# Kernel optimization log

Measured on AMD Instinct MI355X. Metric: run time of the kernel, lower is better.

The kernel has to match this reference:

```python
import jax, jax.numpy as jnp
import numpy as np

K = 1          # self.k: number of hardest positives kept per row
MARGIN = 0.1   # self.margin


def setup_inputs() -> dict:
    key = jax.random.key(0)
    n, d, n_classes = 8192, 512, 1024  # 8 samples per class (balanced, as the torch reshape assumes)
    inputs = jax.random.normal(key, (n, d), dtype=jnp.float32)
    targets = (jnp.arange(n) % n_classes).astype(jnp.int32)
    return {"inputs": inputs, "targets": targets}


def _euclidean_dist(x):
    # ||xi||^2 + ||xj||^2 - 2 xi.xj, clamped then sqrt (matches torch addmm_ version)
    sq = jnp.sum(x * x, axis=1)
    d2 = sq[:, None] + sq[None, :] - 2.0 * (x @ x.T)
    return jnp.sqrt(jnp.clip(d2, 1e-12))


def reference(inputs, targets):
    n = inputs.shape[0]
    dist = _euclidean_dist(inputs)                      # [n, n]

    same = targets[:, None] == targets[None, :]
    eye = jnp.eye(n, dtype=bool)
    pos_mask = same & ~eye                              # same label, excl. diagonal
    neg_mask = ~same                                    # different label

    inf = jnp.asarray(jnp.inf, dist.dtype)
    # per-row sorted positive distances (non-positives pushed to +inf)
    pos_sorted = jnp.sort(jnp.where(pos_mask, dist, inf), axis=1)
    topk_pos = pos_sorted[:, :K]                        # k closest positives per row
    mean_pos = jnp.mean(topk_pos, axis=1)               # mean(pos_pair[:k])
    thresh = pos_sorted[:, K - 1] + MARGIN              # pos_pair[-1] + margin

    # hard negatives: neg distance < threshold
    sel = neg_mask & (dist < thresh[:, None])
    cnt = jnp.sum(sel, axis=1)
    sum_neg = jnp.sum(jnp.where(sel, dist, 0.0), axis=1)
    mean_neg = sum_neg / jnp.maximum(cnt, 1).astype(dist.dtype)

    valid = cnt > 0
    row_loss = jnp.where(valid, mean_pos - mean_neg + MARGIN, 0.0)
    loss = jnp.sum(row_loss) / n

    prec = 1.0 - jnp.sum(valid).astype(dist.dtype) / n
    pos_d = jnp.sum(jnp.where(pos_mask, dist, 0.0)) / jnp.sum(pos_mask).astype(dist.dtype)
    neg_d = jnp.sum(jnp.where(neg_mask, dist, 0.0)) / jnp.sum(neg_mask).astype(dist.dtype)
    return loss, prec, pos_d, neg_d
```

## Files before the change

### kernel.cpp

```cpp
#include <hip/hip_runtime.h>
#include <hip/hip_bf16.h>
#include <math.h>


#define MARGIN_F 0.1f

typedef unsigned short ushort_t;
typedef __attribute__((ext_vector_type(8))) _Float16 f16x8;
typedef __attribute__((ext_vector_type(4))) float f32x4;

__global__ void nl_prep_kernel(const float* __restrict__ x, float* __restrict__ sq,
                               ushort_t* __restrict__ xh,
                               float* __restrict__ neg_total, unsigned int* __restrict__ neg_cnt,
                               int n, int d) {
  int row = blockIdx.x * blockDim.y + threadIdx.y;
  if (row >= n) return;
  const float* xr = x + (size_t)row * d;
  float s = 0.f;
  for (int k = threadIdx.x * 4; k < d; k += 64 * 4) {
    float4 v = *reinterpret_cast<const float4*>(xr + k);
    s = fmaf(v.x, v.x, s); s = fmaf(v.y, v.y, s);
    s = fmaf(v.z, v.z, s); s = fmaf(v.w, v.w, s);
    if (xh != nullptr) {
      float f[4] = {v.x, v.y, v.z, v.w};
      union { ushort_t u[4]; uint2 v2; } H;
#pragma unroll
      for (int t = 0; t < 4; ++t) {
        _Float16 h = (_Float16)f[t];
        H.u[t] = *reinterpret_cast<ushort_t*>(&h);
      }
      *reinterpret_cast<uint2*>(xh + (size_t)row * d + k) = H.v2;
    }
  }
#pragma unroll
  for (int off = 32; off > 0; off >>= 1) s += __shfl_down(s, off, 64);
  if (threadIdx.x == 0) sq[row] = s;
  if (row == 0 && threadIdx.x == 0) { *neg_total = 0.f; *neg_cnt = 0u; }
}

__launch_bounds__(1024)
__global__ void nl_bucket_kernel(const int* __restrict__ targets,
                                 int* __restrict__ cls_start, int* __restrict__ members,
                                 int n) {
  __shared__ int cnt[8192];
  __shared__ int aux[1024];
  const int tid = threadIdx.x;
  for (int k = tid; k < n; k += 1024) cnt[k] = 0;
  __syncthreads();
  for (int k = tid; k < n; k += 1024) atomicAdd(&cnt[targets[k]], 1);
  __syncthreads();
  const int C = (n + 1023) / 1024;
  int v[8]; int s = 0;
  for (int e = 0; e < C; ++e) {
    int idx = tid * C + e;
    int t = (idx < n) ? cnt[idx] : 0;
    v[e] = s; s += t;
  }
  aux[tid] = s;
  __syncthreads();
  for (int off = 1; off < 1024; off <<= 1) {
    int t = (tid >= off) ? aux[tid - off] : 0;
    __syncthreads();
    aux[tid] += t;
    __syncthreads();
  }
  int chunk_excl = aux[tid] - s;
  __syncthreads();
  for (int e = 0; e < C; ++e) {
    int idx = tid * C + e;
    if (idx < n) {
      int st = chunk_excl + v[e];
      cls_start[idx] = st;
      cnt[idx] = st;
    }
  }
  __syncthreads();
  for (int k = tid; k < n; k += 1024) {
    int t = targets[k];
    int p = atomicAdd(&cnt[t], 1);
    members[p] = k;
  }
}

__launch_bounds__(256)
__global__ void nl_pos_bucket(const float* __restrict__ x, const int* __restrict__ targets,
                              const float* __restrict__ sq,
                              const int* __restrict__ cls_start, const int* __restrict__ members,
                              float* __restrict__ min_pos, float* __restrict__ pos_sum,
                              int* __restrict__ pos_cnt,
                              float* __restrict__ sel_sum, int* __restrict__ sel_cnt,
                              int n, int d) {
  const int lane = threadIdx.x & 63;
  const int i = (blockIdx.x * blockDim.x + threadIdx.x) >> 6;
  if (i >= n) return;
  const int tgt = targets[i];
  const float sqi = sq[i];
  const float* xi = x + (size_t)i * d;
  float4 xreg[2];
  const int k0 = lane * 4;
#pragma unroll
  for (int c = 0; c < 2; ++c)
    if (k0 + c * 256 < d) xreg[c] = *reinterpret_cast<const float4*>(xi + k0 + c * 256);
  const int s = cls_start[tgt];
  const int e = (tgt + 1 < n) ? cls_start[tgt + 1] : n;
  float mn = INFINITY, sum = 0.f;
  int cnt = 0;
  for (int mi = s; mi < e; ++mi) {
    int j = members[mi];
    if (j == i) continue;
    const float* xj = x + (size_t)j * d;
    float acc = 0.f;
    if (d == 512) {
      float4 a0 = xreg[0], a1 = xreg[1];
      float4 v0 = *reinterpret_cast<const float4*>(xj + k0);
      float4 v1 = *reinterpret_cast<const float4*>(xj + k0 + 256);
      acc = fmaf(a0.x, v0.x, acc); acc = fmaf(a0.y, v0.y, acc);
      acc = fmaf(a0.z, v0.z, acc); acc = fmaf(a0.w, v0.w, acc);
      acc = fmaf(a1.x, v1.x, acc); acc = fmaf(a1.y, v1.y, acc);
      acc = fmaf(a1.z, v1.z, acc); acc = fmaf(a1.w, v1.w, acc);
    } else {
      for (int k = k0; k < d; k += 256) {
        float4 a = *reinterpret_cast<const float4*>(xi + k);
        float4 v = *reinterpret_cast<const float4*>(xj + k);
        acc = fmaf(a.x, v.x, acc); acc = fmaf(a.y, v.y, acc);
        acc = fmaf(a.z, v.z, acc); acc = fmaf(a.w, v.w, acc);
      }
    }
#pragma unroll
    for (int off = 32; off > 0; off >>= 1) acc += __shfl_down(acc, off, 64);
    if (lane == 0) {
      float d2 = sqi + sq[j] - 2.f * acc;
      float dist = sqrtf(fmaxf(d2, 1e-12f));
      mn = fminf(mn, dist); sum += dist; cnt++;
    }
  }
  if (lane == 0) {
    min_pos[i] = mn; pos_sum[i] = sum; pos_cnt[i] = cnt;
    sel_sum[i] = 0.f; sel_cnt[i] = 0;
  }
}

__launch_bounds__(256)
__global__ void nl_pos_scan(const float* __restrict__ x, const int* __restrict__ targets,
                            const float* __restrict__ sq,
                            float* __restrict__ min_pos, float* __restrict__ pos_sum,
                            int* __restrict__ pos_cnt,
                            float* __restrict__ sel_sum, int* __restrict__ sel_cnt,
                            int n, int d) {
  const int lane = threadIdx.x & 63;
  const int i = (blockIdx.x * blockDim.x + threadIdx.x) >> 6;
  if (i >= n) return;
  const int tgt = targets[i];
  const float sqi = sq[i];
  const float* xi = x + (size_t)i * d;
  float mn = INFINITY, sum = 0.f;
  int cnt = 0;
  for (int j0 = 0; j0 < n; j0 += 64) {
    int j = j0 + lane;
    bool match = (j < n) && (j != i) && (targets[j] == tgt);
    unsigned long long mask = __ballot(match);
    while (mask) {
      int b = __ffsll(mask) - 1;
      mask &= mask - 1;
      int jj = j0 + b;
      const float* xj = x + (size_t)jj * d;
      float acc = 0.f;
      for (int k = lane * 4; k < d; k += 256) {
        float4 a = *reinterpret_cast<const float4*>(xi + k);
        float4 v = *reinterpret_cast<const float4*>(xj + k);
        acc = fmaf(a.x, v.x, acc); acc = fmaf(a.y, v.y, acc);
        acc = fmaf(a.z, v.z, acc); acc = fmaf(a.w, v.w, acc);
      }
#pragma unroll
      for (int off = 32; off > 0; off >>= 1) acc += __shfl_down(acc, off, 64);
      if (lane == 0) {
        float d2 = sqi + sq[jj] - 2.f * acc;
        float dist = sqrtf(fmaxf(d2, 1e-12f));
        mn = fminf(mn, dist); sum += dist; cnt++;
      }
    }
  }
  if (lane == 0) {
    min_pos[i] = mn; pos_sum[i] = sum; pos_cnt[i] = cnt;
    sel_sum[i] = 0.f; sel_cnt[i] = 0;
  }
}

__device__ __forceinline__ void stage_tile(const ushort_t* __restrict__ S, int r0, int k0,
                                           int ld, char* lds) {
  const int tid = threadIdx.x;
#pragma unroll
  for (int i = 0; i < 2; ++i) {
    int c = tid + i * 256;
    int row = c >> 2;
    int kc = (c & 3) ^ ((row >> 1) & 3);
    const ushort_t* g = S + (size_t)(r0 + row) * ld + k0 + kc * 8;
    __builtin_amdgcn_global_load_lds(
        (const __attribute__((address_space(1))) unsigned int*)g,
        (__attribute__((address_space(3))) unsigned int*)(lds + c * 16),
        16, 0, 0);
  }
}

__launch_bounds__(256, 4)
__global__ void nl_main_mfma(const ushort_t* __restrict__ xh,
                             const int* __restrict__ targets, const float* __restrict__ sq,
                             const float* __restrict__ min_pos,
                             float* __restrict__ sel_sum, int* __restrict__ sel_cnt,
                             float* __restrict__ neg_total, unsigned int* __restrict__ neg_cnt,
                             int n, int d) {
  __shared__ char smem[2][2][8192];
  __shared__ float red_sel[128];
  __shared__ int red_cnt[128];
  __shared__ float red_csel[128];
  __shared__ int red_ccnt[128];
  __shared__ float red_neg;
  __shared__ unsigned int red_negc;

  const int tid = threadIdx.x;
  const int lane = tid & 63;
  const int w = tid >> 6;
  const int wr = (w >> 1) & 1, wc = w & 1;

  const int nwg = gridDim.x;
  const int q8 = nwg >> 3, r8 = nwg & 7;
  const int xcd = blockIdx.x & 7, sub = blockIdx.x >> 3;
  const int wg = (xcd < r8 ? xcd * (q8 + 1) : r8 * (q8 + 1) + (xcd - r8) * q8) + sub;

  const int nbx = n >> 7;
  int tt = wg, bi = 0, len = nbx;
  while (tt >= len) { tt -= len; ++bi; --len; }
  const int bj = bi + tt;
  const int row0 = bi * 128, col0 = bj * 128;
  const bool isdiag = (bi == bj);

  if (tid < 128) { red_sel[tid] = 0.f; red_cnt[tid] = 0; red_csel[tid] = 0.f; red_ccnt[tid] = 0; }
  if (tid == 0) { red_neg = 0.f; red_negc = 0u; }

  f32x4 acc[4][4];
#pragma unroll
  for (int m = 0; m < 4; ++m)
#pragma unroll
    for (int nn = 0; nn < 4; ++nn) acc[m][nn] = (f32x4){0.f, 0.f, 0.f, 0.f};

  const int TOT = d >> 5;

  stage_tile(xh, row0, 0, d, smem[0][0]);
  stage_tile(xh, col0, 0, d, smem[0][1]);

  const int r = lane & 15;
  const int g = lane >> 4;
  const int chunk = (g ^ ((r >> 1) & 3)) * 16;

  for (int kt = 0; kt < TOT; ++kt) {
    __builtin_amdgcn_s_barrier();
    __builtin_amdgcn_sched_barrier(0);
    if (kt + 1 < TOT) {
      int k0 = (kt + 1) << 5;
      stage_tile(xh, row0, k0, d, smem[(kt + 1) & 1][0]);
      stage_tile(xh, col0, k0, d, smem[(kt + 1) & 1][1]);
      asm volatile("s_waitcnt vmcnt(4)" ::: "memory");
    } else {
      asm volatile("s_waitcnt vmcnt(0)" ::: "memory");
    }
    __builtin_amdgcn_s_barrier();
    __builtin_amdgcn_sched_barrier(0);

    const char* As = smem[kt & 1][0];
    const char* Bs = smem[kt & 1][1];
    f16x8 a[4], b[4];
#pragma unroll
    for (int m = 0; m < 4; ++m)
      a[m] = *reinterpret_cast<const f16x8*>(As + (wr * 64 + m * 16 + r) * 64 + chunk);
#pragma unroll
    for (int nn = 0; nn < 4; ++nn)
      b[nn] = *reinterpret_cast<const f16x8*>(Bs + (wc * 64 + nn * 16 + r) * 64 + chunk);
#pragma unroll
    for (int m = 0; m < 4; ++m)
#pragma unroll
      for (int nn = 0; nn < 4; ++nn)
        acc[m][nn] = __builtin_amdgcn_mfma_f32_16x16x32_f16(a[m], b[nn], acc[m][nn], 0, 0, 0);
  }

  const int col_base = col0 + wc * 64;
  float sqj[4], thrj[4];
  int tgtj[4];
#pragma unroll
  for (int nn = 0; nn < 4; ++nn) {
    int gc = col_base + nn * 16 + (lane & 15);
    sqj[nn] = sq[gc];
    tgtj[nn] = targets[gc];
    thrj[nn] = min_pos[gc] + MARGIN_F;
  }
  float negsum = 0.f;
  unsigned int negc = 0u;
  float colsum[4] = {0.f, 0.f, 0.f, 0.f};
  int colcnt[4] = {0, 0, 0, 0};
#pragma unroll
  for (int m = 0; m < 4; ++m) {
#pragma unroll
    for (int reg = 0; reg < 4; ++reg) {
      int lrow = wr * 64 + m * 16 + (lane >> 4) * 4 + reg;
      int gr = row0 + lrow;
      float sqi = sq[gr];
      int tgti = targets[gr];
      float thr = min_pos[gr] + MARGIN_F;
      float rs = 0.f; int rc = 0;
#pragma unroll
      for (int nn = 0; nn < 4; ++nn) {
        float d2 = sqi + sqj[nn] - 2.f * acc[m][nn][reg];
        float dist = sqrtf(fmaxf(d2, 1e-12f));
        if (tgti != tgtj[nn]) {
          negsum += dist; negc++;
          if (dist < thr) { rc++; rs += dist; }
          if (!isdiag && dist < thrj[nn]) { colcnt[nn]++; colsum[nn] += dist; }
        }
      }
#pragma unroll
      for (int off = 1; off < 16; off <<= 1) {
        rs += __shfl_xor(rs, off, 64);
        rc += __shfl_xor(rc, off, 64);
      }
      if ((lane & 15) == 0) {
        atomicAdd(&red_cnt[lrow], rc);
        atomicAdd(&red_sel[lrow], rs);
      }
    }
  }
  if (!isdiag) {
#pragma unroll
    for (int nn = 0; nn < 4; ++nn) {
      float cs = colsum[nn]; int cc = colcnt[nn];
      cs += __shfl_xor(cs, 16, 64); cc += __shfl_xor(cc, 16, 64);
      cs += __shfl_xor(cs, 32, 64); cc += __shfl_xor(cc, 32, 64);
      if ((lane >> 4) == 0 && cc) {
        int lcol = wc * 64 + nn * 16 + lane;
        atomicAdd(&red_ccnt[lcol], cc);
        atomicAdd(&red_csel[lcol], cs);
      }
    }
    negsum *= 2.f; negc *= 2u;
  }
#pragma unroll
  for (int off = 32; off > 0; off >>= 1) {
    negsum += __shfl_down(negsum, off, 64);
    negc += __shfl_down(negc, off, 64);
  }
  if (lane == 0) { atomicAdd(&red_neg, negsum); atomicAdd(&red_negc, negc); }
  __syncthreads();
  if (tid < 128) {
    int c = red_cnt[tid];
    if (c > 0) {
      atomicAdd(&sel_cnt[row0 + tid], c);
      atomicAdd(&sel_sum[row0 + tid], red_sel[tid]);
    }
    if (!isdiag) {
      int c2 = red_ccnt[tid];
      if (c2 > 0) {
        atomicAdd(&sel_cnt[col0 + tid], c2);
        atomicAdd(&sel_sum[col0 + tid], red_csel[tid]);
      }
    }
  }
  if (tid == 0) { atomicAdd(neg_total, red_neg); atomicAdd(neg_cnt, red_negc); }
}

#define BM 128
#define BN 128
#define BK 16
#define PAD 4
__launch_bounds__(256)
__global__ void nl_main_kernel(const float* __restrict__ x, const int* __restrict__ targets,
                               const float* __restrict__ sq, const float* __restrict__ min_pos,
                               float* __restrict__ sel_sum, int* __restrict__ sel_cnt,
                               float* __restrict__ neg_total, unsigned int* __restrict__ neg_cnt,
                               int n, int d) {
  __shared__ float As[BK][BM + PAD];
  __shared__ float Bs[BK][BN + PAD];
  __shared__ float red_sel[BM];
  __shared__ int red_cnt[BM];
  __shared__ float red_neg;
  __shared__ unsigned int red_negc;

  const int tid = threadIdx.x;
  const int tx = tid & 15;
  const int ty = tid >> 4;
  const int row0 = blockIdx.y * BM;
  const int col0 = blockIdx.x * BN;

  if (tid < BM) { red_sel[tid] = 0.f; red_cnt[tid] = 0; }
  if (tid == 0) { red_neg = 0.f; red_negc = 0u; }

  float acc[8][8];
#pragma unroll
  for (int i = 0; i < 8; ++i)
#pragma unroll
    for (int j = 0; j < 8; ++j) acc[i][j] = 0.f;

  const int lr = tid >> 2;
  const int lk = (tid & 3) << 2;

  for (int k0 = 0; k0 < d; k0 += BK) {
    float4 va0 = *reinterpret_cast<const float4*>(x + (size_t)(row0 + lr) * d + k0 + lk);
    float4 va1 = *reinterpret_cast<const float4*>(x + (size_t)(row0 + lr + 64) * d + k0 + lk);
    float4 vb0 = *reinterpret_cast<const float4*>(x + (size_t)(col0 + lr) * d + k0 + lk);
    float4 vb1 = *reinterpret_cast<const float4*>(x + (size_t)(col0 + lr + 64) * d + k0 + lk);
    __syncthreads();
    As[lk + 0][lr] = va0.x; As[lk + 1][lr] = va0.y; As[lk + 2][lr] = va0.z; As[lk + 3][lr] = va0.w;
    As[lk + 0][lr + 64] = va1.x; As[lk + 1][lr + 64] = va1.y; As[lk + 2][lr + 64] = va1.z; As[lk + 3][lr + 64] = va1.w;
    Bs[lk + 0][lr] = vb0.x; Bs[lk + 1][lr] = vb0.y; Bs[lk + 2][lr] = vb0.z; Bs[lk + 3][lr] = vb0.w;
    Bs[lk + 0][lr + 64] = vb1.x; Bs[lk + 1][lr + 64] = vb1.y; Bs[lk + 2][lr + 64] = vb1.z; Bs[lk + 3][lr + 64] = vb1.w;
    __syncthreads();
#pragma unroll
    for (int k = 0; k < BK; ++k) {
      float a[8], b[8];
      *reinterpret_cast<float4*>(&a[0]) = *reinterpret_cast<const float4*>(&As[k][ty * 4]);
      *reinterpret_cast<float4*>(&a[4]) = *reinterpret_cast<const float4*>(&As[k][ty * 4 + 64]);
      *reinterpret_cast<float4*>(&b[0]) = *reinterpret_cast<const float4*>(&Bs[k][tx * 4]);
      *reinterpret_cast<float4*>(&b[4]) = *reinterpret_cast<const float4*>(&Bs[k][tx * 4 + 64]);
#pragma unroll
      for (int mm = 0; mm < 8; ++mm)
#pragma unroll
        for (int nn = 0; nn < 8; ++nn)
          acc[mm][nn] = fmaf(a[mm], b[nn], acc[mm][nn]);
    }
  }

  float sqj[8]; int tgtj[8];
#pragma unroll
  for (int nn = 0; nn < 8; ++nn) {
    int lc = tx * 4 + (nn & 3) + ((nn >> 2) << 6);
    sqj[nn] = sq[col0 + lc];
    tgtj[nn] = targets[col0 + lc];
  }
  float negsum = 0.f;
  unsigned int negc = 0u;
#pragma unroll
  for (int mm = 0; mm < 8; ++mm) {
    int lrow = ty * 4 + (mm & 3) + ((mm >> 2) << 6);
    int gi = row0 + lrow;
    float sqi = sq[gi];
    int tgti = targets[gi];
    float thr = min_pos[gi] + MARGIN_F;
    float rs = 0.f; int rc = 0;
#pragma unroll
    for (int nn = 0; nn < 8; ++nn) {
      float d2 = sqi + sqj[nn] - 2.f * acc[mm][nn];
      float dist = sqrtf(fmaxf(d2, 1e-12f));
      if (tgti != tgtj[nn]) {
        negsum += dist; negc++;
        if (dist < thr) { rc++; rs += dist; }
      }
    }
    if (rc) { atomicAdd(&red_cnt[lrow], rc); atomicAdd(&red_sel[lrow], rs); }
  }
#pragma unroll
  for (int off = 32; off > 0; off >>= 1) {
    negsum += __shfl_down(negsum, off, 64);
    negc += __shfl_down(negc, off, 64);
  }
  if ((tid & 63) == 0) { atomicAdd(&red_neg, negsum); atomicAdd(&red_negc, negc); }
  __syncthreads();
  if (tid < BM && red_cnt[tid] > 0) {
    atomicAdd(&sel_cnt[row0 + tid], red_cnt[tid]);
    atomicAdd(&sel_sum[row0 + tid], red_sel[tid]);
  }
  if (tid == 0) { atomicAdd(neg_total, red_neg); atomicAdd(neg_cnt, red_negc); }
}

__global__ void nl_finalize(const float* __restrict__ min_pos, const float* __restrict__ pos_sum,
                            const int* __restrict__ pos_cnt, const float* __restrict__ sel_sum,
                            const int* __restrict__ sel_cnt, const float* __restrict__ neg_total,
                            const unsigned int* __restrict__ neg_cnt, float* __restrict__ out,
                            int n) {
  const int tid = threadIdx.x;
  float loss = 0.f, psum = 0.f;
  int nvalid = 0, pcnt = 0;
  for (int i = tid; i < n; i += 256) {
    int c = sel_cnt[i];
    if (c > 0) {
      float mean_neg = sel_sum[i] / (float)c;
      loss += min_pos[i] - mean_neg + MARGIN_F;
      nvalid++;
    }
    psum += pos_sum[i];
    pcnt += pos_cnt[i];
  }
  __shared__ float s_loss[256];
  __shared__ float s_psum[256];
  __shared__ int s_nv[256];
  __shared__ int s_pc[256];
  s_loss[tid] = loss; s_psum[tid] = psum; s_nv[tid] = nvalid; s_pc[tid] = pcnt;
  __syncthreads();
  for (int s = 128; s > 0; s >>= 1) {
    if (tid < s) {
      s_loss[tid] += s_loss[tid + s];
      s_psum[tid] += s_psum[tid + s];
      s_nv[tid] += s_nv[tid + s];
      s_pc[tid] += s_pc[tid + s];
    }
    __syncthreads();
  }
  if (tid == 0) {
    out[0] = s_loss[0] / (float)n;
    out[1] = 1.f - (float)s_nv[0] / (float)n;
    out[2] = s_psum[0] / (float)s_pc[0];
    out[3] = neg_total[0] / (float)neg_cnt[0];
  }
}

extern "C" void kernel_launch(void* const* d_in, const int* in_sizes, int n_in,
                              void* d_out, int out_size, void* d_ws, size_t ws_size,
                              hipStream_t stream) {
  const float* x = (const float*)d_in[0];
  const int* targets = (const int*)d_in[1];
  float* out = (float*)d_out;
  const int n = in_sizes[1];
  const int d = in_sizes[0] / n;

  float* sq = (float*)d_ws;
  float* min_pos = sq + n;
  float* pos_sum = min_pos + n;
  int* pos_cnt = (int*)(pos_sum + n);
  float* sel_sum = (float*)(pos_cnt + n);
  int* sel_cnt = (int*)(sel_sum + n);
  int* cls_start = (int*)(sel_cnt + n);
  int* members = cls_start + n;
  float* neg_total = (float*)(members + n);
  unsigned int* neg_cnt = (unsigned int*)(neg_total + 1);
  size_t stats_bytes = ((size_t)(8 * n + 2) * 4 + 255) & ~(size_t)255;
  ushort_t* xh = (ushort_t*)((char*)d_ws + stats_bytes);
  size_t need = stats_bytes + (size_t)n * d * sizeof(ushort_t);

  const bool mfma_ok = (ws_size >= need) && (n % 128) == 0 && (d % 32) == 0;
  const bool bucket_ok = (ws_size >= stats_bytes) && (n <= 8192) && (d % 16) == 0;

  nl_prep_kernel<<<dim3((n + 3) / 4), dim3(64, 4), 0, stream>>>(
      x, sq, mfma_ok ? xh : nullptr, neg_total, neg_cnt, n, d);
  if (bucket_ok) {
    nl_bucket_kernel<<<1, 1024, 0, stream>>>(targets, cls_start, members, n);
    nl_pos_bucket<<<(n * 64 + 255) / 256, 256, 0, stream>>>(
        x, targets, sq, cls_start, members, min_pos, pos_sum, pos_cnt, sel_sum, sel_cnt, n, d);
  } else {
    nl_pos_scan<<<(n * 64 + 255) / 256, 256, 0, stream>>>(
        x, targets, sq, min_pos, pos_sum, pos_cnt, sel_sum, sel_cnt, n, d);
  }

  if (mfma_ok) {
    int nbx = n / 128;
    int ntiles = nbx * (nbx + 1) / 2;
    nl_main_mfma<<<ntiles, 256, 0, stream>>>(xh, targets, sq, min_pos, sel_sum,
                                             sel_cnt, neg_total, neg_cnt, n, d);
  } else {
    nl_main_kernel<<<dim3(n / BN, n / BM), 256, 0, stream>>>(x, targets, sq, min_pos, sel_sum,
                                                             sel_cnt, neg_total, neg_cnt, n, d);
  }
  nl_finalize<<<1, 256, 0, stream>>>(min_pos, pos_sum, pos_cnt, sel_sum, sel_cnt,
                                     neg_total, neg_cnt, out, n);
}
```

Measured before the change: 175.3 us.

## Fold bucketing into prep kernel and finalize in last MFMA block

The class-bucketing step moves into block 0 of the prep kernel, now run with 256 threads instead of a separate 1024-thread launch. The finalize reduction moves into the tail of the MFMA kernel: the last block to finish, found with a global done counter, does it. This removes two kernel launches and their gaps. In exchange, prep block 0 takes longer and carries 32KB of shared memory, and every MFMA block pays a threadfence plus an atomic on the counter.

```diff
diff --git a/kernel.cpp b/kernel.cpp
--- a/kernel.cpp
+++ b/kernel.cpp
@@ -11,74 +11,77 @@
 
 __global__ void nl_prep_kernel(const float* __restrict__ x, float* __restrict__ sq,
                                ushort_t* __restrict__ xh,
+                               const int* __restrict__ targets,
+                               int* __restrict__ cls_start, int* __restrict__ members,
                                float* __restrict__ neg_total, unsigned int* __restrict__ neg_cnt,
-                               int n, int d) {
+                               unsigned int* __restrict__ done_ctr,
+                               int n, int d, int do_bucket) {
+  __shared__ int cnt[8192];
+  __shared__ int aux2[256];
   int row = blockIdx.x * blockDim.y + threadIdx.y;
-  if (row >= n) return;
-  const float* xr = x + (size_t)row * d;
-  float s = 0.f;
-  for (int k = threadIdx.x * 4; k < d; k += 64 * 4) {
-    float4 v = *reinterpret_cast<const float4*>(xr + k);
-    s = fmaf(v.x, v.x, s); s = fmaf(v.y, v.y, s);
-    s = fmaf(v.z, v.z, s); s = fmaf(v.w, v.w, s);
-    if (xh != nullptr) {
-      float f[4] = {v.x, v.y, v.z, v.w};
-      union { ushort_t u[4]; uint2 v2; } H;
-#pragma unroll
-      for (int t = 0; t < 4; ++t) {
-        _Float16 h = (_Float16)f[t];
-        H.u[t] = *reinterpret_cast<ushort_t*>(&h);
-      }
-      *reinterpret_cast<uint2*>(xh + (size_t)row * d + k) = H.v2;
-    }
-  }
-#pragma unroll
-  for (int off = 32; off > 0; off >>= 1) s += __shfl_down(s, off, 64);
-  if (threadIdx.x == 0) sq[row] = s;
-  if (row == 0 && threadIdx.x == 0) { *neg_total = 0.f; *neg_cnt = 0u; }
-}
-
-__launch_bounds__(1024)
-__global__ void nl_bucket_kernel(const int* __restrict__ targets,
-                                 int* __restrict__ cls_start, int* __restrict__ members,
-                                 int n) {
-  __shared__ int cnt[8192];
-  __shared__ int aux[1024];
-  const int tid = threadIdx.x;
-  for (int k = tid; k < n; k += 1024) cnt[k] = 0;
-  __syncthreads();
-  for (int k = tid; k < n; k += 1024) atomicAdd(&cnt[targets[k]], 1);
-  __syncthreads();
-  const int C = (n + 1023) / 1024;
-  int v[8]; int s = 0;
-  for (int e = 0; e < C; ++e) {
-    int idx = tid * C + e;
-    int t = (idx < n) ? cnt[idx] : 0;
-    v[e] = s; s += t;
-  }
-  aux[tid] = s;
-  __syncthreads();
-  for (int off = 1; off < 1024; off <<= 1) {
-    int t = (tid >= off) ? aux[tid - off] : 0;
-    __syncthreads();
-    aux[tid] += t;
-    __syncthreads();
-  }
-  int chunk_excl = aux[tid] - s;
-  __syncthreads();
-  for (int e = 0; e < C; ++e) {
-    int idx = tid * C + e;
-    if (idx < n) {
-      int st = chunk_excl + v[e];
-      cls_start[idx] = st;
-      cnt[idx] = st;
-    }
-  }
-  __syncthreads();
-  for (int k = tid; k < n; k += 1024) {
-    int t = targets[k];
-    int p = atomicAdd(&cnt[t], 1);
-    members[p] = k;
+  if (row < n) {
+    const float* xr = x + (size_t)row * d;
+    float s = 0.f;
+    for (int k = threadIdx.x * 4; k < d; k += 64 * 4) {
+      float4 v = *reinterpret_cast<const float4*>(xr + k);
+      s = fmaf(v.x, v.x, s); s = fmaf(v.y, v.y, s);
+      s = fmaf(v.z, v.z, s); s = fmaf(v.w, v.w, s);
+      if (xh != nullptr) {
+        float f[4] = {v.x, v.y, v.z, v.w};
+        union { ushort_t u[4]; uint2 v2; } H;
+#pragma unroll
+        for (int t = 0; t < 4; ++t) {
+          _Float16 h = (_Float16)f[t];
+          H.u[t] = *reinterpret_cast<ushort_t*>(&h);
+        }
+        *reinterpret_cast<uint2*>(xh + (size_t)row * d + k) = H.v2;
+      }
+    }
+#pragma unroll
+    for (int off = 32; off > 0; off >>= 1) s += __shfl_down(s, off, 64);
+    if (threadIdx.x == 0) sq[row] = s;
+    if (row == 0 && threadIdx.x == 0) {
+      *neg_total = 0.f; *neg_cnt = 0u; *done_ctr = 0u;
+    }
+  }
+
+  if (do_bucket && blockIdx.x == 0) {
+    const int tid = threadIdx.y * 64 + threadIdx.x;
+    for (int k = tid; k < n; k += 256) cnt[k] = 0;
+    __syncthreads();
+    for (int k = tid; k < n; k += 256) atomicAdd(&cnt[targets[k]], 1);
+    __syncthreads();
+    const int C = (n + 255) / 256;
+    int s = 0;
+    for (int e = 0; e < C; ++e) {
+      int idx = tid * C + e;
+      if (idx < n) s += cnt[idx];
+    }
+    aux2[tid] = s;
+    __syncthreads();
+    for (int off = 1; off < 256; off <<= 1) {
+      int t = (tid >= off) ? aux2[tid - off] : 0;
+      __syncthreads();
+      aux2[tid] += t;
+      __syncthreads();
+    }
+    int run = aux2[tid] - s;
+    __syncthreads();
+    for (int e = 0; e < C; ++e) {
+      int idx = tid * C + e;
+      if (idx < n) {
+        int t = cnt[idx];
+        cls_start[idx] = run;
+        cnt[idx] = run;
+        run += t;
+      }
+    }
+    __syncthreads();
+    for (int k = tid; k < n; k += 256) {
+      int t = targets[k];
+      int p = atomicAdd(&cnt[t], 1);
+      members[p] = k;
+    }
   }
 }
 
@@ -206,8 +209,10 @@
 __global__ void nl_main_mfma(const ushort_t* __restrict__ xh,
                              const int* __restrict__ targets, const float* __restrict__ sq,
                              const float* __restrict__ min_pos,
+                             const float* __restrict__ pos_sum, const int* __restrict__ pos_cnt,
                              float* __restrict__ sel_sum, int* __restrict__ sel_cnt,
                              float* __restrict__ neg_total, unsigned int* __restrict__ neg_cnt,
+                             unsigned int* __restrict__ done_ctr, float* __restrict__ out,
                              int n, int d) {
   __shared__ char smem[2][2][8192];
   __shared__ float red_sel[128];
@@ -216,6 +221,9 @@
   __shared__ int red_ccnt[128];
   __shared__ float red_neg;
   __shared__ unsigned int red_negc;
+  __shared__ int amLast;
+  __shared__ float w_loss[4], w_psum[4];
+  __shared__ int w_nv[4], w_pc[4];
 
   const int tid = threadIdx.x;
   const int lane = tid & 63;
@@ -363,6 +371,47 @@
     }
   }
   if (tid == 0) { atomicAdd(neg_total, red_neg); atomicAdd(neg_cnt, red_negc); }
+
+  __threadfence();
+  if (tid == 0) {
+    unsigned int old = atomicAdd(done_ctr, 1u);
+    amLast = (old == (unsigned int)(gridDim.x - 1));
+  }
+  __syncthreads();
+  if (amLast) {
+    float loss = 0.f, psum = 0.f;
+    int nvalid = 0, pcnt = 0;
+    for (int i = tid; i < n; i += 256) {
+      int c = __hip_atomic_load(&sel_cnt[i], __ATOMIC_RELAXED, __HIP_MEMORY_SCOPE_AGENT);
+      float ss = __hip_atomic_load(&sel_sum[i], __ATOMIC_RELAXED, __HIP_MEMORY_SCOPE_AGENT);
+      if (c > 0) {
+        loss += min_pos[i] - ss / (float)c + MARGIN_F;
+        nvalid++;
+      }
+      psum += pos_sum[i];
+      pcnt += pos_cnt[i];
+    }
+#pragma unroll
+    for (int off = 32; off > 0; off >>= 1) {
+      loss += __shfl_down(loss, off, 64);
+      psum += __shfl_down(psum, off, 64);
+      nvalid += __shfl_down(nvalid, off, 64);
+      pcnt += __shfl_down(pcnt, off, 64);
+    }
+    if (lane == 0) { w_loss[w] = loss; w_psum[w] = psum; w_nv[w] = nvalid; w_pc[w] = pcnt; }
+    __syncthreads();
+    if (tid == 0) {
+      float L = 0.f, P = 0.f; int NV = 0, PC = 0;
+#pragma unroll
+      for (int k = 0; k < 4; ++k) { L += w_loss[k]; P += w_psum[k]; NV += w_nv[k]; PC += w_pc[k]; }
+      float ngt = __hip_atomic_load(neg_total, __ATOMIC_RELAXED, __HIP_MEMORY_SCOPE_AGENT);
+      unsigned int ngc = __hip_atomic_load(neg_cnt, __ATOMIC_RELAXED, __HIP_MEMORY_SCOPE_AGENT);
+      out[0] = L / (float)n;
+      out[1] = 1.f - (float)NV / (float)n;
+      out[2] = P / (float)PC;
+      out[3] = ngt / (float)ngc;
+    }
+  }
 }
 
 #define BM 128
@@ -528,7 +577,8 @@
   int* members = cls_start + n;
   float* neg_total = (float*)(members + n);
   unsigned int* neg_cnt = (unsigned int*)(neg_total + 1);
-  size_t stats_bytes = ((size_t)(8 * n + 2) * 4 + 255) & ~(size_t)255;
+  unsigned int* done_ctr = neg_cnt + 1;
+  size_t stats_bytes = ((size_t)(8 * n + 8) * 4 + 255) & ~(size_t)255;
   ushort_t* xh = (ushort_t*)((char*)d_ws + stats_bytes);
   size_t need = stats_bytes + (size_t)n * d * sizeof(ushort_t);
 
@@ -536,9 +586,9 @@
   const bool bucket_ok = (ws_size >= stats_bytes) && (n <= 8192) && (d % 16) == 0;
 
   nl_prep_kernel<<<dim3((n + 3) / 4), dim3(64, 4), 0, stream>>>(
-      x, sq, mfma_ok ? xh : nullptr, neg_total, neg_cnt, n, d);
+      x, sq, mfma_ok ? xh : nullptr, targets, cls_start, members,
+      neg_total, neg_cnt, done_ctr, n, d, bucket_ok ? 1 : 0);
   if (bucket_ok) {
-    nl_bucket_kernel<<<1, 1024, 0, stream>>>(targets, cls_start, members, n);
     nl_pos_bucket<<<(n * 64 + 255) / 256, 256, 0, stream>>>(
         x, targets, sq, cls_start, members, min_pos, pos_sum, pos_cnt, sel_sum, sel_cnt, n, d);
   } else {
@@ -549,12 +599,13 @@
   if (mfma_ok) {
     int nbx = n / 128;
     int ntiles = nbx * (nbx + 1) / 2;
-    nl_main_mfma<<<ntiles, 256, 0, stream>>>(xh, targets, sq, min_pos, sel_sum,
-                                             sel_cnt, neg_total, neg_cnt, n, d);
+    nl_main_mfma<<<ntiles, 256, 0, stream>>>(xh, targets, sq, min_pos, pos_sum, pos_cnt,
+                                             sel_sum, sel_cnt, neg_total, neg_cnt,
+                                             done_ctr, out, n, d);
   } else {
     nl_main_kernel<<<dim3(n / BN, n / BM), 256, 0, stream>>>(x, targets, sq, min_pos, sel_sum,
                                                              sel_cnt, neg_total, neg_cnt, n, d);
-  }
-  nl_finalize<<<1, 256, 0, stream>>>(min_pos, pos_sum, pos_cnt, sel_sum, sel_cnt,
-                                     neg_total, neg_cnt, out, n);
-}
+    nl_finalize<<<1, 256, 0, stream>>>(min_pos, pos_sum, pos_cnt, sel_sum, sel_cnt,
+                                       neg_total, neg_cnt, out, n);
+  }
+}
```

Measured after the change: 316.3 us. +80.4%, slower.
